# Kernel tuning notes

Measured on AMD Instinct MI355X. Metric: run time of the kernel, lower is better.

The kernel has to match this reference:

```python
import jax, jax.numpy as jnp
import numpy as np

NORM = 1.0  # normalization_factor


def _glorot(key, shape):
    fan_in, fan_out = shape
    lim = float(np.sqrt(6.0 / (fan_in + fan_out)))
    return jax.random.uniform(key, shape, jnp.float32, -lim, lim)


def setup_inputs() -> dict:
    key = jax.random.key(0)
    ks = jax.random.split(key, 12)
    B, N = 8, 2048
    latent, hidden, out_dim = 64, 128, 64
    inp = {
        "latent_features": jax.random.normal(ks[0], (B, N, latent), jnp.float32),
        "adjacency_matrix": jax.random.uniform(ks[1], (B, N, N), jnp.float32),
        "node_mask": jnp.ones((B, N, 1), jnp.float32),
        # 3 GCN layers: latent->hidden, hidden->hidden, hidden->hidden
        "W0": _glorot(ks[2], (latent, hidden)), "b0": jnp.zeros((hidden,), jnp.float32),
        "W1": _glorot(ks[3], (hidden, hidden)), "b1": jnp.zeros((hidden,), jnp.float32),
        "W2": _glorot(ks[4], (hidden, hidden)), "b2": jnp.zeros((hidden,), jnp.float32),
        # output projection hidden->out_dim
        "Wout": _glorot(ks[5], (hidden, out_dim)), "bout": jnp.zeros((out_dim,), jnp.float32),
    }
    return inp


def _gcn_layer(h, adj, W, b):
    # message transform (linear), gather+sum aggregate via dense adjacency, ReLU act
    msg = h @ W + b                      # [B,N,dout]
    agg = jnp.einsum('bij,bjd->bid', adj, msg) / NORM  # sum aggregation over neighbors
    return jax.nn.relu(agg)


def reference(latent_features, adjacency_matrix, node_mask,
              W0, b0, W1, b1, W2, b2, Wout, bout):
    h = _gcn_layer(latent_features, adjacency_matrix, W0, b0)
    h = _gcn_layer(h, adjacency_matrix, W1, b1)
    h = _gcn_layer(h, adjacency_matrix, W2, b2)
    # output projection + node mask
    return (h @ Wout + bout) * node_mask
```

## Files before the change

kernel.cpp:

```cpp
#include <hip/hip_runtime.h>
#include <hip/hip_bf16.h>


typedef __bf16 bf16;
typedef __bf16 bf16x4 __attribute__((ext_vector_type(4)));
typedef __bf16 bf16x8 __attribute__((ext_vector_type(8)));
typedef float  f32x16 __attribute__((ext_vector_type(16)));
typedef float  f32x4  __attribute__((ext_vector_type(4)));

static __device__ inline f32x16 mfma32(bf16x8 a, bf16x8 b, f32x16 c) {
    return __builtin_amdgcn_mfma_f32_32x32x16_bf16(a, b, c, 0, 0, 0);
}

#define NB   8
#define NN   2048
#define LAT  64
#define HID  128
#define ODIM 64

__global__ __launch_bounds__(256) void prep_k(
    const float* __restrict__ W0, const float* __restrict__ W1,
    const float* __restrict__ W2, const float* __restrict__ Wout,
    bf16* __restrict__ WT0, bf16* __restrict__ WT1,
    bf16* __restrict__ WT2, bf16* __restrict__ WoutT)
{
    int i = blockIdx.x * 256 + threadIdx.x;
    if (i < HID * LAT) {
        int fo = i >> 6, k = i & 63;
        WT0[i] = (bf16)W0[k * HID + fo]; return;
    }
    i -= HID * LAT;
    if (i < HID * HID) {
        int fo = i >> 7, k = i & 127;
        WT1[i] = (bf16)W1[k * HID + fo]; return;
    }
    i -= HID * HID;
    if (i < HID * HID) {
        int fo = i >> 7, k = i & 127;
        WT2[i] = (bf16)W2[k * HID + fo]; return;
    }
    i -= HID * HID;
    if (i < ODIM * HID) {
        int o = i >> 7, k = i & 127;
        WoutT[i] = (bf16)Wout[k * ODIM + o]; return;
    }
}

__global__ __launch_bounds__(256) void transform0_k(
    const float* __restrict__ lat, const bf16* __restrict__ WT0,
    const float* __restrict__ b0, bf16* __restrict__ msgT)
{
    int tid = threadIdx.x;
    int l = tid & 63, w = tid >> 6;
    int lm = l & 31, lh = l >> 5;
    int g0 = blockIdx.x * 64;
    int b  = g0 >> 11, nb = g0 & 2047;

    const bf16*  Wrow = WT0 + (size_t)(w * 32 + lm) * LAT + lh * 8;
    const float* r0   = lat + (size_t)(g0 + lm) * LAT + lh * 8;
    const float* r1   = r0 + (size_t)32 * LAT;

    f32x16 acc0 = {}, acc1 = {};
    for (int k0 = 0; k0 < LAT; k0 += 16) {
        bf16x8 a  = *(const bf16x8*)(Wrow + k0);
        f32x4 x0 = *(const f32x4*)(r0 + k0), x1 = *(const f32x4*)(r0 + k0 + 4);
        f32x4 y0 = *(const f32x4*)(r1 + k0), y1 = *(const f32x4*)(r1 + k0 + 4);
        bf16x8 v0, v1;
        v0[0]=(bf16)x0[0]; v0[1]=(bf16)x0[1]; v0[2]=(bf16)x0[2]; v0[3]=(bf16)x0[3];
        v0[4]=(bf16)x1[0]; v0[5]=(bf16)x1[1]; v0[6]=(bf16)x1[2]; v0[7]=(bf16)x1[3];
        v1[0]=(bf16)y0[0]; v1[1]=(bf16)y0[1]; v1[2]=(bf16)y0[2]; v1[3]=(bf16)y0[3];
        v1[4]=(bf16)y1[0]; v1[5]=(bf16)y1[1]; v1[6]=(bf16)y1[2]; v1[7]=(bf16)y1[3];
        acc0 = mfma32(a, v0, acc0);
        acc1 = mfma32(a, v1, acc1);
    }

    bf16* outb = msgT + (size_t)b * (HID * NN) + nb;
#pragma unroll
    for (int r = 0; r < 16; ++r) {
        int fo = w * 32 + (r & 3) + 8 * (r >> 2) + 4 * lh;
        float bv = b0[fo];
        outb[(size_t)fo * NN + lm]      = (bf16)(acc0[r] + bv);
        outb[(size_t)fo * NN + 32 + lm] = (bf16)(acc1[r] + bv);
    }
}

template<int MODE>
__global__ __launch_bounds__(256) void agg_fused_k(
    const float* __restrict__ adj, const bf16* __restrict__ msgT,
    const bf16* __restrict__ WTn, const float* __restrict__ biasn,
    bf16* __restrict__ msg_out, const float* __restrict__ mask,
    float* __restrict__ out)
{
    __shared__ __align__(16) bf16 As[2][32 * 72];
    __shared__ __align__(16) bf16 Bs[2][128 * 72];
    __shared__ __align__(16) bf16 Hs[32 * 136];
    int tid = threadIdx.x;
    int l = tid & 63, w = tid >> 6;
    int lm = l & 31, lh = l >> 5;
    int b  = blockIdx.x >> 6;
    int m0 = (blockIdx.x & 63) * 32;

    const float* adjb = adj + (size_t)b * NN * NN + (size_t)m0 * NN;
    const bf16*  msgb = msgT + (size_t)b * (HID * NN);

    int ar = tid >> 4, ac = (tid & 15) * 4;
    const float* asrc = adjb + (size_t)ar * NN + ac;
    int br = tid >> 3, bc = (tid & 7) * 8;
    const bf16* bsrc = msgb + (size_t)br * NN + bc;

    f32x4 pa0, pa1;
    bf16x8 pb0, pb1, pb2, pb3;

    pa0 = *(const f32x4*)(asrc);
    pa1 = *(const f32x4*)(asrc + (size_t)16 * NN);
    pb0 = *(const bf16x8*)(bsrc);
    pb1 = *(const bf16x8*)(bsrc + (size_t)32 * NN);
    pb2 = *(const bf16x8*)(bsrc + (size_t)64 * NN);
    pb3 = *(const bf16x8*)(bsrc + (size_t)96 * NN);
    {
        bf16x4 va0, va1;
        va0[0]=(bf16)pa0[0]; va0[1]=(bf16)pa0[1]; va0[2]=(bf16)pa0[2]; va0[3]=(bf16)pa0[3];
        va1[0]=(bf16)pa1[0]; va1[1]=(bf16)pa1[1]; va1[2]=(bf16)pa1[2]; va1[3]=(bf16)pa1[3];
        *(bf16x4*)&As[0][ar * 72 + ac]        = va0;
        *(bf16x4*)&As[0][(ar + 16) * 72 + ac] = va1;
        *(bf16x8*)&Bs[0][br * 72 + bc]        = pb0;
        *(bf16x8*)&Bs[0][(br + 32) * 72 + bc] = pb1;
        *(bf16x8*)&Bs[0][(br + 64) * 72 + bc] = pb2;
        *(bf16x8*)&Bs[0][(br + 96) * 72 + bc] = pb3;
    }
    __syncthreads();

    f32x16 acc = {};
    for (int kt = 0; kt < 32; ++kt) {
        int cur = kt & 1;
        bool more = kt < 31;
        int k1 = (kt + 1) * 64;
        if (more) {
            pa0 = *(const f32x4*)(asrc + k1);
            pa1 = *(const f32x4*)(asrc + (size_t)16 * NN + k1);
            pb0 = *(const bf16x8*)(bsrc + k1);
            pb1 = *(const bf16x8*)(bsrc + (size_t)32 * NN + k1);
            pb2 = *(const bf16x8*)(bsrc + (size_t)64 * NN + k1);
            pb3 = *(const bf16x8*)(bsrc + (size_t)96 * NN + k1);
        }
        const bf16* Ac = &As[cur][lm * 72 + lh * 8];
        const bf16* Bc = &Bs[cur][(w * 32 + lm) * 72 + lh * 8];
#pragma unroll
        for (int s = 0; s < 4; ++s)
            acc = mfma32(*(const bf16x8*)(Ac + s * 16), *(const bf16x8*)(Bc + s * 16), acc);
        if (more) {
            int nxt = cur ^ 1;
            bf16x4 va0, va1;
            va0[0]=(bf16)pa0[0]; va0[1]=(bf16)pa0[1]; va0[2]=(bf16)pa0[2]; va0[3]=(bf16)pa0[3];
            va1[0]=(bf16)pa1[0]; va1[1]=(bf16)pa1[1]; va1[2]=(bf16)pa1[2]; va1[3]=(bf16)pa1[3];
            *(bf16x4*)&As[nxt][ar * 72 + ac]        = va0;
            *(bf16x4*)&As[nxt][(ar + 16) * 72 + ac] = va1;
            *(bf16x8*)&Bs[nxt][br * 72 + bc]        = pb0;
            *(bf16x8*)&Bs[nxt][(br + 32) * 72 + bc] = pb1;
            *(bf16x8*)&Bs[nxt][(br + 64) * 72 + bc] = pb2;
            *(bf16x8*)&Bs[nxt][(br + 96) * 72 + bc] = pb3;
        }
        __syncthreads();
    }

#pragma unroll
    for (int r = 0; r < 16; ++r) {
        int row = (r & 3) + 8 * (r >> 2) + 4 * lh;
        float v = acc[r];
        Hs[row * 136 + w * 32 + lm] = (bf16)(v > 0.f ? v : 0.f);
    }
    __syncthreads();

    if (MODE == 0) {
        const bf16* Arow = WTn + (size_t)(w * 32 + lm) * HID + lh * 8;
        const bf16* Brow = &Hs[lm * 136 + lh * 8];
        f32x16 acc2 = {};
#pragma unroll
        for (int s = 0; s < 8; ++s)
            acc2 = mfma32(*(const bf16x8*)(Arow + s * 16), *(const bf16x8*)(Brow + s * 16), acc2);
        bf16* outb = msg_out + (size_t)b * (HID * NN) + m0;
#pragma unroll
        for (int r = 0; r < 16; ++r) {
            int fo = w * 32 + (r & 3) + 8 * (r >> 2) + 4 * lh;
            outb[(size_t)fo * NN + lm] = (bf16)(acc2[r] + biasn[fo]);
        }
    } else {
        if (w < 2) {
            int ob = w * 32;
            const bf16* Arow = &Hs[lm * 136 + lh * 8];
            const bf16* Brow = WTn + (size_t)(ob + lm) * HID + lh * 8;
            f32x16 acc2 = {};
#pragma unroll
            for (int s = 0; s < 8; ++s)
                acc2 = mfma32(*(const bf16x8*)(Arow + s * 16), *(const bf16x8*)(Brow + s * 16), acc2);
            float bv = biasn[ob + lm];
#pragma unroll
            for (int r = 0; r < 16; ++r) {
                int node = (r & 3) + 8 * (r >> 2) + 4 * lh;
                int g = b * NN + m0 + node;
                out[(size_t)g * ODIM + ob + lm] = (acc2[r] + bv) * mask[g];
            }
        }
    }
}

extern "C" void kernel_launch(void* const* d_in, const int* in_sizes, int n_in,
                              void* d_out, int out_size, void* d_ws, size_t ws_size,
                              hipStream_t stream)
{
    const float* lat  = (const float*)d_in[0];
    const float* adj  = (const float*)d_in[1];
    const float* mask = (const float*)d_in[2];
    const float* W0   = (const float*)d_in[3];
    const float* b0   = (const float*)d_in[4];
    const float* W1   = (const float*)d_in[5];
    const float* b1   = (const float*)d_in[6];
    const float* W2   = (const float*)d_in[7];
    const float* b2   = (const float*)d_in[8];
    const float* Wout = (const float*)d_in[9];
    const float* bout = (const float*)d_in[10];
    float* out = (float*)d_out;

    char* ws = (char*)d_ws;
    bf16* msgA  = (bf16*)(ws + 0);
    bf16* msgB  = (bf16*)(ws + 4194304);
    bf16* WT0   = (bf16*)(ws + 8388608);
    bf16* WT1   = (bf16*)(ws + 8404992);
    bf16* WT2   = (bf16*)(ws + 8437760);
    bf16* WoutT = (bf16*)(ws + 8470528);

    prep_k<<<192, 256, 0, stream>>>(W0, W1, W2, Wout, WT0, WT1, WT2, WoutT);

    transform0_k<<<256, 256, 0, stream>>>(lat, WT0, b0, msgA);
    agg_fused_k<0><<<512, 256, 0, stream>>>(adj, msgA, WT1, b1, msgB, nullptr, nullptr);
    agg_fused_k<0><<<512, 256, 0, stream>>>(adj, msgB, WT2, b2, msgA, nullptr, nullptr);
    agg_fused_k<1><<<512, 256, 0, stream>>>(adj, msgA, WoutT, bout, nullptr, mask, out);
}
```

Before: 331.8 us.

## Cache bf16 adjacency in first pass and reuse it in later layers

The first aggregation kernel converts the fp32 adjacency to bf16 and writes that copy to workspace. The second and third layers then read the half-size bf16 copy instead of fp32. Weight prep and the first transform are fused into one launch with W0 transposed in shared memory. The block index is remapped so batch varies fastest, and the K loop uses two register sets for prefetching. The cost is an extra 64MB write in the first pass and a much larger workspace.

```diff
diff --git a/kernel.cpp b/kernel.cpp
--- a/kernel.cpp
+++ b/kernel.cpp
@@ -18,51 +18,47 @@
 #define HID  128
 #define ODIM 64
 
-__global__ __launch_bounds__(256) void prep_k(
-    const float* __restrict__ W0, const float* __restrict__ W1,
-    const float* __restrict__ W2, const float* __restrict__ Wout,
-    bf16* __restrict__ WT0, bf16* __restrict__ WT1,
+__global__ __launch_bounds__(256) void prep_t0_k(
+    const float* __restrict__ lat, const float* __restrict__ W0,
+    const float* __restrict__ b0,
+    const float* __restrict__ W1, const float* __restrict__ W2,
+    const float* __restrict__ Wout,
+    bf16* __restrict__ msgT, bf16* __restrict__ WT1,
     bf16* __restrict__ WT2, bf16* __restrict__ WoutT)
 {
-    int i = blockIdx.x * 256 + threadIdx.x;
-    if (i < HID * LAT) {
-        int fo = i >> 6, k = i & 63;
-        WT0[i] = (bf16)W0[k * HID + fo]; return;
-    }
-    i -= HID * LAT;
-    if (i < HID * HID) {
-        int fo = i >> 7, k = i & 127;
-        WT1[i] = (bf16)W1[k * HID + fo]; return;
-    }
-    i -= HID * HID;
-    if (i < HID * HID) {
-        int fo = i >> 7, k = i & 127;
-        WT2[i] = (bf16)W2[k * HID + fo]; return;
-    }
-    i -= HID * HID;
-    if (i < ODIM * HID) {
-        int o = i >> 7, k = i & 127;
-        WoutT[i] = (bf16)Wout[k * ODIM + o]; return;
-    }
-}
-
-__global__ __launch_bounds__(256) void transform0_k(
-    const float* __restrict__ lat, const bf16* __restrict__ WT0,
-    const float* __restrict__ b0, bf16* __restrict__ msgT)
-{
+    __shared__ __align__(16) bf16 WTs[HID * 72];
     int tid = threadIdx.x;
+    int blk = blockIdx.x;
+
+    if (blk >= 256) {
+        int i = (blk - 256) * 256 + tid;
+        if (i < HID * HID) { int fo = i >> 7, k = i & 127; WT1[i] = (bf16)W1[k * HID + fo]; return; }
+        i -= HID * HID;
+        if (i < HID * HID) { int fo = i >> 7, k = i & 127; WT2[i] = (bf16)W2[k * HID + fo]; return; }
+        i -= HID * HID;
+        if (i < ODIM * HID) { int o = i >> 7, k = i & 127; WoutT[i] = (bf16)Wout[k * ODIM + o]; return; }
+        return;
+    }
+
+    for (int i = tid; i < LAT * HID; i += 256) {
+        int k = i >> 7, fo = i & 127;
+        WTs[fo * 72 + k] = (bf16)W0[i];
+    }
+    __syncthreads();
+
     int l = tid & 63, w = tid >> 6;
     int lm = l & 31, lh = l >> 5;
-    int g0 = blockIdx.x * 64;
+    int g0 = blk * 64;
     int b  = g0 >> 11, nb = g0 & 2047;
 
-    const bf16*  Wrow = WT0 + (size_t)(w * 32 + lm) * LAT + lh * 8;
+    const bf16*  Wrow = &WTs[(w * 32 + lm) * 72 + lh * 8];
     const float* r0   = lat + (size_t)(g0 + lm) * LAT + lh * 8;
     const float* r1   = r0 + (size_t)32 * LAT;
 
     f32x16 acc0 = {}, acc1 = {};
+#pragma unroll
     for (int k0 = 0; k0 < LAT; k0 += 16) {
-        bf16x8 a  = *(const bf16x8*)(Wrow + k0);
+        bf16x8 a = *(const bf16x8*)(Wrow + k0);
         f32x4 x0 = *(const f32x4*)(r0 + k0), x1 = *(const f32x4*)(r0 + k0 + 4);
         f32x4 y0 = *(const f32x4*)(r1 + k0), y1 = *(const f32x4*)(r1 + k0 + 4);
         bf16x8 v0, v1;
@@ -84,12 +80,13 @@
     }
 }
 
-template<int MODE>
-__global__ __launch_bounds__(256) void agg_fused_k(
-    const float* __restrict__ adj, const bf16* __restrict__ msgT,
-    const bf16* __restrict__ WTn, const float* __restrict__ biasn,
-    bf16* __restrict__ msg_out, const float* __restrict__ mask,
-    float* __restrict__ out)
+template<int MODE, int ADJW>
+__global__ __launch_bounds__(256) void agg_k(
+    const float* __restrict__ adjf, const bf16* __restrict__ adjbi,
+    bf16* __restrict__ adjbo,
+    const bf16* __restrict__ msgT, const bf16* __restrict__ WTn,
+    const float* __restrict__ biasn, bf16* __restrict__ msg_out,
+    const float* __restrict__ mask, float* __restrict__ out)
 {
     __shared__ __align__(16) bf16 As[2][32 * 72];
     __shared__ __align__(16) bf16 Bs[2][128 * 72];
@@ -97,69 +94,76 @@
     int tid = threadIdx.x;
     int l = tid & 63, w = tid >> 6;
     int lm = l & 31, lh = l >> 5;
-    int b  = blockIdx.x >> 6;
-    int m0 = (blockIdx.x & 63) * 32;
-
-    const float* adjb = adj + (size_t)b * NN * NN + (size_t)m0 * NN;
-    const bf16*  msgb = msgT + (size_t)b * (HID * NN);
-
-    int ar = tid >> 4, ac = (tid & 15) * 4;
-    const float* asrc = adjb + (size_t)ar * NN + ac;
+    int b  = blockIdx.x & 7;
+    int m0 = (blockIdx.x >> 3) * 32;
+
+    const bf16* msgb = msgT + (size_t)b * (HID * NN);
     int br = tid >> 3, bc = (tid & 7) * 8;
     const bf16* bsrc = msgb + (size_t)br * NN + bc;
 
-    f32x4 pa0, pa1;
-    bf16x8 pb0, pb1, pb2, pb3;
-
-    pa0 = *(const f32x4*)(asrc);
-    pa1 = *(const f32x4*)(asrc + (size_t)16 * NN);
-    pb0 = *(const bf16x8*)(bsrc);
-    pb1 = *(const bf16x8*)(bsrc + (size_t)32 * NN);
-    pb2 = *(const bf16x8*)(bsrc + (size_t)64 * NN);
-    pb3 = *(const bf16x8*)(bsrc + (size_t)96 * NN);
-    {
-        bf16x4 va0, va1;
-        va0[0]=(bf16)pa0[0]; va0[1]=(bf16)pa0[1]; va0[2]=(bf16)pa0[2]; va0[3]=(bf16)pa0[3];
-        va1[0]=(bf16)pa1[0]; va1[1]=(bf16)pa1[1]; va1[2]=(bf16)pa1[2]; va1[3]=(bf16)pa1[3];
-        *(bf16x4*)&As[0][ar * 72 + ac]        = va0;
-        *(bf16x4*)&As[0][(ar + 16) * 72 + ac] = va1;
-        *(bf16x8*)&Bs[0][br * 72 + bc]        = pb0;
-        *(bf16x8*)&Bs[0][(br + 32) * 72 + bc] = pb1;
-        *(bf16x8*)&Bs[0][(br + 64) * 72 + bc] = pb2;
-        *(bf16x8*)&Bs[0][(br + 96) * 72 + bc] = pb3;
-    }
-    __syncthreads();
+    int ar = tid >> 4, ac = (tid & 15) * 4;
+    const float* asrc = (ADJW == 0) ? adjf + (size_t)b * NN * NN + (size_t)(m0 + ar) * NN + ac : nullptr;
+    bf16* adst = (ADJW == 0) ? adjbo + (size_t)b * NN * NN + (size_t)(m0 + ar) * NN + ac : nullptr;
+    int ar8 = tid >> 3, ac8 = (tid & 7) * 8;
+    const bf16* asrcb = (ADJW == 1) ? adjbi + (size_t)b * NN * NN + (size_t)(m0 + ar8) * NN + ac8 : nullptr;
+
+    f32x4  fa0[2], fa1[2];
+    bf16x8 ba[2];
+    bf16x8 pb[2][4];
+
+    auto loadTile = [&](int set, int k) {
+        if (ADJW == 0) {
+            fa0[set] = *(const f32x4*)(asrc + k);
+            fa1[set] = *(const f32x4*)(asrc + (size_t)16 * NN + k);
+        } else {
+            ba[set] = *(const bf16x8*)(asrcb + k);
+        }
+        pb[set][0] = *(const bf16x8*)(bsrc + k);
+        pb[set][1] = *(const bf16x8*)(bsrc + (size_t)32 * NN + k);
+        pb[set][2] = *(const bf16x8*)(bsrc + (size_t)64 * NN + k);
+        pb[set][3] = *(const bf16x8*)(bsrc + (size_t)96 * NN + k);
+    };
+    auto storeTile = [&](int set, int buf, int k) {
+        if (ADJW == 0) {
+            bf16x4 v0, v1;
+            v0[0]=(bf16)fa0[set][0]; v0[1]=(bf16)fa0[set][1]; v0[2]=(bf16)fa0[set][2]; v0[3]=(bf16)fa0[set][3];
+            v1[0]=(bf16)fa1[set][0]; v1[1]=(bf16)fa1[set][1]; v1[2]=(bf16)fa1[set][2]; v1[3]=(bf16)fa1[set][3];
+            *(bf16x4*)&As[buf][ar * 72 + ac]        = v0;
+            *(bf16x4*)&As[buf][(ar + 16) * 72 + ac] = v1;
+            *(bf16x4*)(adst + k)                    = v0;
+            *(bf16x4*)(adst + (size_t)16 * NN + k)  = v1;
+        } else {
+            *(bf16x8*)&As[buf][ar8 * 72 + ac8] = ba[set];
+        }
+        *(bf16x8*)&Bs[buf][br * 72 + bc]        = pb[set][0];
+        *(bf16x8*)&Bs[buf][(br + 32) * 72 + bc] = pb[set][1];
+        *(bf16x8*)&Bs[buf][(br + 64) * 72 + bc] = pb[set][2];
+        *(bf16x8*)&Bs[buf][(br + 96) * 72 + bc] = pb[set][3];
+    };
 
     f32x16 acc = {};
-    for (int kt = 0; kt < 32; ++kt) {
-        int cur = kt & 1;
-        bool more = kt < 31;
-        int k1 = (kt + 1) * 64;
-        if (more) {
-            pa0 = *(const f32x4*)(asrc + k1);
-            pa1 = *(const f32x4*)(asrc + (size_t)16 * NN + k1);
-            pb0 = *(const bf16x8*)(bsrc + k1);
-            pb1 = *(const bf16x8*)(bsrc + (size_t)32 * NN + k1);
-            pb2 = *(const bf16x8*)(bsrc + (size_t)64 * NN + k1);
-            pb3 = *(const bf16x8*)(bsrc + (size_t)96 * NN + k1);
-        }
-        const bf16* Ac = &As[cur][lm * 72 + lh * 8];
-        const bf16* Bc = &Bs[cur][(w * 32 + lm) * 72 + lh * 8];
+    auto mfmaTile = [&](int buf) {
+        const bf16* Ac = &As[buf][lm * 72 + lh * 8];
+        const bf16* Bc = &Bs[buf][(w * 32 + lm) * 72 + lh * 8];
 #pragma unroll
         for (int s = 0; s < 4; ++s)
             acc = mfma32(*(const bf16x8*)(Ac + s * 16), *(const bf16x8*)(Bc + s * 16), acc);
-        if (more) {
-            int nxt = cur ^ 1;
-            bf16x4 va0, va1;
-            va0[0]=(bf16)pa0[0]; va0[1]=(bf16)pa0[1]; va0[2]=(bf16)pa0[2]; va0[3]=(bf16)pa0[3];
-            va1[0]=(bf16)pa1[0]; va1[1]=(bf16)pa1[1]; va1[2]=(bf16)pa1[2]; va1[3]=(bf16)pa1[3];
-            *(bf16x4*)&As[nxt][ar * 72 + ac]        = va0;
-            *(bf16x4*)&As[nxt][(ar + 16) * 72 + ac] = va1;
-            *(bf16x8*)&Bs[nxt][br * 72 + bc]        = pb0;
-            *(bf16x8*)&Bs[nxt][(br + 32) * 72 + bc] = pb1;
-            *(bf16x8*)&Bs[nxt][(br + 64) * 72 + bc] = pb2;
-            *(bf16x8*)&Bs[nxt][(br + 96) * 72 + bc] = pb3;
-        }
+    };
+
+    loadTile(0, 0);
+    loadTile(1, 64);
+    storeTile(0, 0, 0);
+    __syncthreads();
+
+#pragma unroll 1
+    for (int kt = 0; kt < 32; kt += 2) {
+        if (kt + 2 < 32) loadTile(0, (kt + 2) * 64);
+        mfmaTile(0);
+        storeTile(1, 1, (kt + 1) * 64);
+        __syncthreads();
+        if (kt + 3 < 32) loadTile(1, (kt + 3) * 64);
+        mfmaTile(1);
+        if (kt + 2 < 32) storeTile(0, 0, (kt + 2) * 64);
         __syncthreads();
     }
 
@@ -224,15 +228,14 @@
     char* ws = (char*)d_ws;
     bf16* msgA  = (bf16*)(ws + 0);
     bf16* msgB  = (bf16*)(ws + 4194304);
-    bf16* WT0   = (bf16*)(ws + 8388608);
-    bf16* WT1   = (bf16*)(ws + 8404992);
-    bf16* WT2   = (bf16*)(ws + 8437760);
-    bf16* WoutT = (bf16*)(ws + 8470528);
-
-    prep_k<<<192, 256, 0, stream>>>(W0, W1, W2, Wout, WT0, WT1, WT2, WoutT);
-
-    transform0_k<<<256, 256, 0, stream>>>(lat, WT0, b0, msgA);
-    agg_fused_k<0><<<512, 256, 0, stream>>>(adj, msgA, WT1, b1, msgB, nullptr, nullptr);
-    agg_fused_k<0><<<512, 256, 0, stream>>>(adj, msgB, WT2, b2, msgA, nullptr, nullptr);
-    agg_fused_k<1><<<512, 256, 0, stream>>>(adj, msgA, WoutT, bout, nullptr, mask, out);
-}
+    bf16* adjbf = (bf16*)(ws + 8388608);
+    bf16* WT1   = (bf16*)(ws + 75497472);
+    bf16* WT2   = (bf16*)(ws + 75530240);
+    bf16* WoutT = (bf16*)(ws + 75563008);
+
+    prep_t0_k<<<416, 256, 0, stream>>>(lat, W0, b0, W1, W2, Wout, msgA, WT1, WT2, WoutT);
+
+    agg_k<0, 0><<<512, 256, 0, stream>>>(adj, nullptr, adjbf, msgA, WT1, b1, msgB, nullptr, nullptr);
+    agg_k<0, 1><<<512, 256, 0, stream>>>(nullptr, adjbf, nullptr, msgB, WT2, b2, msgA, nullptr, nullptr);
+    agg_k<1, 1><<<512, 256, 0, stream>>>(nullptr, adjbf, nullptr, msgA, WoutT, bout, nullptr, mask, out);
+}
```

New measurement: 284.4 us. 1.17x faster.
